# Kernel optimization log

Hardware: AMD Instinct MI355X
Metric: run time of the kernel (lower is better)

## Reference

```python
import jax, jax.numpy as jnp
import numpy as np

EPS = 1e-9  # Dice BatchNorm epsilon

def _dice(x, alpha, mm, mv):
    # Keras BN(center=False, scale=False) in inference mode: (x - moving_mean) / sqrt(moving_var + eps)
    p = jax.nn.sigmoid((x - mm) * jax.lax.rsqrt(mv + EPS))
    return x * (p + alpha * (1.0 - p))

def setup_inputs() -> dict:
    key = jax.random.key(0)
    ks = jax.random.split(key, 8)
    B, T, E = 4096, 200, 12
    return {
        "query": jax.random.normal(ks[0], (B, 1, E), jnp.float32),
        "keys": jax.random.normal(ks[1], (B, T, E), jnp.float32),
        "mask": jnp.ones((B, T), dtype=bool),
        "W0": jax.random.normal(ks[2], (48, 80), jnp.float32) * (1.0 / np.sqrt(48)),
        "b0": jnp.zeros((80,), jnp.float32),
        "W1": jax.random.normal(ks[3], (80, 40), jnp.float32) * (1.0 / np.sqrt(80)),
        "b1": jnp.zeros((40,), jnp.float32),
        "alpha0": jax.random.uniform(ks[4], (80,), jnp.float32),
        "alpha1": jax.random.uniform(ks[5], (40,), jnp.float32),
        "mm0": jnp.zeros((80,), jnp.float32),
        "mv0": jnp.ones((80,), jnp.float32),
        "mm1": jnp.zeros((40,), jnp.float32),
        "mv1": jnp.ones((40,), jnp.float32),
        "atten_kernel": jax.random.normal(ks[6], (40, 1), jnp.float32) * (1.0 / np.sqrt(40)),
        "atten_bias": jnp.zeros((1,), jnp.float32),
    }

def reference(query, keys, mask, W0, b0, W1, b1, alpha0, alpha1,
              mm0, mv0, mm1, mv1, atten_kernel, atten_bias):
    B, T, E = keys.shape
    q = jnp.broadcast_to(query, (B, T, E))  # K.repeat_elements(query, T, 1)
    att = jnp.concatenate([q, keys, q - keys, q * keys], axis=-1)  # [B, T, 4E=48]
    h = _dice(jnp.einsum('bti,io->bto', att, W0) + b0, alpha0, mm0, mv0)  # [B,T,80]
    h = _dice(jnp.einsum('bti,io->bto', h, W1) + b1, alpha1, mm1, mv1)    # [B,T,40]
    score = jnp.einsum('bti,io->bto', h, atten_kernel) + atten_bias       # [B,T,1]
    scores = jnp.swapaxes(score, 1, 2)  # [B,1,T]
    # NOTE: original code computes tf.where(mask,...) but overwrites it and
    # matmuls the UNMASKED scores with keys (bug reproduced faithfully).
    return jnp.matmul(scores, keys)  # [B,1,E]
```

## Files before the change

kernel.cpp:

```cpp
#include <hip/hip_runtime.h>
#include <hip/hip_bf16.h>
#include <math.h>

#define B_TOT 4096
#define T_LEN 200
#define E_DIM 12
#define LOG2E 1.44269504088896340736f

typedef __attribute__((ext_vector_type(8))) short bf16x8;
typedef __attribute__((ext_vector_type(4))) float f32x4;
typedef unsigned short ushort_t;


__device__ inline unsigned short f2bf(float f) {
    union { float f; unsigned u; } x; x.f = f;
    unsigned r = x.u + 0x7FFFu + ((x.u >> 16) & 1u);
    return (unsigned short)(r >> 16);
}
__device__ inline unsigned pk_bf16(float a, float b) {
    float2 t; t.x = a; t.y = b;
    __hip_bfloat162 h = __float22bfloat162_rn(t);
    union { __hip_bfloat162 h; unsigned u; } cv; cv.h = h;
    return cv.u;
}

__global__ __launch_bounds__(256) void din_prep(
    const float* __restrict__ W0, const float* __restrict__ b0v,
    const float* __restrict__ W1, const float* __restrict__ b1v,
    const float* __restrict__ a0, const float* __restrict__ a1,
    const float* __restrict__ mm0, const float* __restrict__ mv0,
    const float* __restrict__ mm1, const float* __restrict__ mv1,
    const float* __restrict__ ak, const float* __restrict__ ab,
    void* __restrict__ wsv)
{
    unsigned char* wsb = (unsigned char*)wsv;
    ushort_t* w0e2 = (ushort_t*)wsb;
    ushort_t* wq   = (ushort_t*)(wsb + 5120);
    ushort_t* w1e  = (ushort_t*)(wsb + 10240);
    float* d0c = (float*)(wsb + 19456);
    float* d1c = (float*)(wsb + 20736);

    int idx = blockIdx.x * 256 + threadIdx.x;
    if (idx < 2560) {
        int n = idx >> 5, k = idx & 31;
        float v = 0.0f;
        if (k < 12)       v = W0[(12 + k) * 80 + n] - W0[(24 + k) * 80 + n];
        else if (k < 24)  v = W0[(36 + (k - 12)) * 80 + n];
        w0e2[n * 32 + k] = f2bf(v);
    } else if (idx < 5120) {
        int v2 = idx - 2560;
        int n = v2 >> 5, k = v2 & 31;
        float v = 0.0f;
        if (k < 12)       v = W0[k * 80 + n] + W0[(24 + k) * 80 + n];
        else if (k == 12) v = b0v[n];
        wq[n * 32 + k] = f2bf(v);
    } else if (idx < 9728) {
        int v2 = idx - 5120;
        int n = v2 / 96, k = v2 - n * 96;
        float v = 0.0f;
        if (n < 40) {
            if (k < 80)       v = W1[k * 40 + n];
            else if (k == 80) v = b1v[n];
        } else if (n == 40 && k == 80) {
            v = 1.0f;
        }
        w1e[n * 96 + k] = f2bf(v);
    } else if (idx < 10048) {
        int v2 = idx - 9728;
        int o = v2 >> 2, c = v2 & 3;
        float rs = rsqrtf(mv0[o] + 1e-9f) * LOG2E;
        float val = (c == 0) ? -rs : (c == 1) ? mm0[o] * rs : (c == 2) ? a0[o] : 1.0f - a0[o];
        d0c[o * 4 + c] = val;
    } else {
        int v2 = idx - 10048;
        int j = v2 >> 2, c = v2 & 3;
        float val = 0.0f;
        if (j < 40) {
            float rs = rsqrtf(mv1[j] + 1e-9f) * LOG2E;
            val = (c == 0) ? -rs : (c == 1) ? mm1[j] * rs : (c == 2) ? a1[j] * ak[j]
                                                          : (1.0f - a1[j]) * ak[j];
        } else if (j == 40 && c == 2) {
            val = ab[0];
        }
        d1c[j * 4 + c] = val;
    }
}

#define A0_STR 40
#define H_STR  104
#define W1_STR 104
#define W0_STR 40

__global__ __launch_bounds__(256, 3) void din_mfma(
    const float* __restrict__ query, const float* __restrict__ keys,
    const void* __restrict__ wsv, float* __restrict__ out)
{
    __shared__ __align__(16) ushort_t Aseg[4 * 64];
    __shared__ __align__(16) ushort_t A0[4 * 64 * A0_STR];
    __shared__ __align__(16) ushort_t H[4 * 16 * H_STR];
    __shared__ __align__(16) f32x4 d0cL[80];
    __shared__ __align__(16) f32x4 d1cL[48];
    __shared__ __align__(16) ushort_t w1eL[48 * W1_STR];
    __shared__ __align__(16) ushort_t w0e2L[80 * W0_STR];
    const unsigned char* wsb = (const unsigned char*)wsv;
    const ushort_t* w0e2 = (const ushort_t*)wsb;
    const ushort_t* wq   = (const ushort_t*)(wsb + 5120);
    const ushort_t* w1e  = (const ushort_t*)(wsb + 10240);
    const f32x4* d0cp = (const f32x4*)(wsb + 19456);
    const f32x4* d1cp = (const f32x4*)(wsb + 20736);

    const int tid = threadIdx.x;
    const int lane = tid & 63;
    const int w = tid >> 6;
    const int l15 = lane & 15;
    const int quad = lane >> 4;
    const int b = blockIdx.x * 4 + w;

    ushort_t* A0w = &A0[w * 64 * A0_STR];
    ushort_t* Hw  = &H[w * 16 * H_STR];
    ushort_t* Asw = &Aseg[w * 64];

    if (tid < 80)        d0cL[tid] = d0cp[tid];
    else if (tid < 128)  d1cL[tid - 80] = d1cp[tid - 80];
    for (int idx = tid; idx < 48 * 12; idx += 256) {
        int row = idx / 12, g = idx - row * 12;
        *(uint4*)(w1eL + row * W1_STR + g * 8) =
            *(const uint4*)(w1e + row * 96 + g * 8);
    }
    for (int idx = tid; idx < 80 * 4; idx += 256) {
        int row = idx >> 2, g = idx & 3;
        *(uint4*)(w0e2L + row * W0_STR + g * 8) =
            *(const uint4*)(w0e2 + row * 32 + g * 8);
    }

    float qq[12];
    {
        const float4* qp = (const float4*)(query + (size_t)b * E_DIM);
        float4 q0 = qp[0], q1 = qp[1], q2 = qp[2];
        qq[0]=q0.x; qq[1]=q0.y; qq[2]=q0.z; qq[3]=q0.w;
        qq[4]=q1.x; qq[5]=q1.y; qq[6]=q1.z; qq[7]=q1.w;
        qq[8]=q2.x; qq[9]=q2.y; qq[10]=q2.z; qq[11]=q2.w;
    }

    float z0q[5];
    {
        unsigned p01 = pk_bf16(qq[0], qq[1]), p23 = pk_bf16(qq[2], qq[3]);
        unsigned p45 = pk_bf16(qq[4], qq[5]), p67 = pk_bf16(qq[6], qq[7]);
        unsigned p89 = pk_bf16(qq[8], qq[9]), pab = pk_bf16(qq[10], qq[11]);
        union { unsigned u[4]; bf16x8 v; } qa;
        qa.u[0] = (quad == 0) ? p01 : (quad == 1) ? p89 : 0u;
        qa.u[1] = (quad == 0) ? p23 : (quad == 1) ? pab : 0u;
        qa.u[2] = (quad == 0) ? p45 : (quad == 1) ? 0x00003F80u : 0u;
        qa.u[3] = (quad == 0) ? p67 : 0u;
        #pragma unroll
        for (int nt = 0; nt < 5; ++nt) {
            bf16x8 wf = *(const bf16x8*)(wq + (nt * 16 + l15) * 32 + quad * 8);
            f32x4 zz = {0.f, 0.f, 0.f, 0.f};
            zz = __builtin_amdgcn_mfma_f32_16x16x32_bf16(qa.v, wf, zz, 0, 0, 0);
            z0q[nt] = zz[0];
        }
    }

    if (quad == 0) {
        bf16x8 one8 = {(short)0x3F80, 0, 0, 0, 0, 0, 0, 0};
        bf16x8 zero8 = {0, 0, 0, 0, 0, 0, 0, 0};
        *(bf16x8*)(Hw + l15 * H_STR + 80) = one8;
        *(bf16x8*)(Hw + l15 * H_STR + 88) = zero8;
    }
    {
        uint4 z4; z4.x = 0u; z4.y = 0u; z4.z = 0u; z4.w = 0u;
        ((uint4*)(A0w + lane * A0_STR))[3] = z4;
    }

    __syncthreads();

    f32x4 acc2 = {0.f, 0.f, 0.f, 0.f};

    for (int c = 0; c < 4; ++c) {
        const int t0 = c * 64;
        const int myT = t0 + lane;
        const bool valid = myT < T_LEN;

        float kk[12];
        if (valid) {
            const float4* kp = (const float4*)(keys + ((size_t)b * T_LEN + myT) * E_DIM);
            float4 k0 = kp[0], k1 = kp[1], k2 = kp[2];
            kk[0]=k0.x; kk[1]=k0.y; kk[2]=k0.z; kk[3]=k0.w;
            kk[4]=k1.x; kk[5]=k1.y; kk[6]=k1.z; kk[7]=k1.w;
            kk[8]=k2.x; kk[9]=k2.y; kk[10]=k2.z; kk[11]=k2.w;
        } else {
            #pragma unroll
            for (int i = 0; i < 12; ++i) kk[i] = 0.0f;
        }
        {
            unsigned kw[6], qkw[6];
            #pragma unroll
            for (int i = 0; i < 6; ++i)
                kw[i] = pk_bf16(kk[2 * i], kk[2 * i + 1]);
            #pragma unroll
            for (int i = 0; i < 6; ++i)
                qkw[i] = pk_bf16(qq[2 * i] * kk[2 * i], qq[2 * i + 1] * kk[2 * i + 1]);
            uint4* dst = (uint4*)(A0w + lane * A0_STR);
            uint4 v0, v1, v2;
            v0.x = kw[0];  v0.y = kw[1];  v0.z = kw[2];  v0.w = kw[3];
            v1.x = kw[4];  v1.y = kw[5];  v1.z = qkw[0]; v1.w = qkw[1];
            v2.x = qkw[2]; v2.y = qkw[3]; v2.z = qkw[4]; v2.w = qkw[5];
            dst[0] = v0; dst[1] = v1; dst[2] = v2;
        }

        const int ntiles = (c < 3) ? 4 : 1;
        for (int ti = 0; ti < ntiles; ++ti) {
            bf16x8 a0 = *(const bf16x8*)(A0w + (ti * 16 + l15) * A0_STR + quad * 8);

            #pragma unroll
            for (int nt = 0; nt < 5; ++nt) {
                bf16x8 b0 = *(const bf16x8*)(w0e2L + (nt * 16 + l15) * W0_STR + quad * 8);
                float zq = z0q[nt];
                f32x4 cc = {zq, zq, zq, zq};
                cc = __builtin_amdgcn_mfma_f32_16x16x32_bf16(a0, b0, cc, 0, 0, 0);
                f32x4 dc = d0cL[nt * 16 + l15];
                float h[4];
                #pragma unroll
                for (int r = 0; r < 4; ++r) {
                    float z = cc[r];
                    float pg = __builtin_amdgcn_rcpf(
                        1.0f + __builtin_amdgcn_exp2f(fmaf(z, dc.x, dc.y)));
                    h[r] = z * fmaf(pg, dc.w, dc.z);
                }
                unsigned u01 = pk_bf16(h[0], h[1]);
                unsigned u23 = pk_bf16(h[2], h[3]);
                ushort_t* hcol = Hw + (quad * 4) * H_STR + nt * 16 + l15;
                hcol[0 * H_STR] = (ushort_t)u01;
                hcol[1 * H_STR] = (ushort_t)(u01 >> 16);
                hcol[2 * H_STR] = (ushort_t)u23;
                hcol[3 * H_STR] = (ushort_t)(u23 >> 16);
            }

            bf16x8 af[3];
            #pragma unroll
            for (int ks = 0; ks < 3; ++ks)
                af[ks] = *(const bf16x8*)(Hw + l15 * H_STR + ks * 32 + quad * 8);
            float s[4] = {0.f, 0.f, 0.f, 0.f};
            #pragma unroll
            for (int nt = 0; nt < 3; ++nt) {
                f32x4 cc = {0.f, 0.f, 0.f, 0.f};
                #pragma unroll
                for (int ks = 0; ks < 3; ++ks) {
                    bf16x8 bf = *(const bf16x8*)(w1eL + (nt * 16 + l15) * W1_STR
                                                 + ks * 32 + quad * 8);
                    cc = __builtin_amdgcn_mfma_f32_16x16x32_bf16(af[ks], bf, cc, 0, 0, 0);
                }
                f32x4 dc1 = d1cL[nt * 16 + l15];
                #pragma unroll
                for (int r = 0; r < 4; ++r) {
                    float z = cc[r];
                    float pg = __builtin_amdgcn_rcpf(
                        1.0f + __builtin_amdgcn_exp2f(fmaf(z, dc1.x, dc1.y)));
                    s[r] = fmaf(z, fmaf(pg, dc1.w, dc1.z), s[r]);
                }
            }
            #pragma unroll
            for (int m = 1; m < 16; m <<= 1) {
                #pragma unroll
                for (int r = 0; r < 4; ++r) s[r] += __shfl_xor(s[r], m, 64);
            }
            if (l15 == 0) {
                const int tb = t0 + ti * 16 + quad * 4;
                float v0 = (tb + 0 < T_LEN) ? s[0] : 0.0f;
                float v1 = (tb + 1 < T_LEN) ? s[1] : 0.0f;
                float v2 = (tb + 2 < T_LEN) ? s[2] : 0.0f;
                float v3 = (tb + 3 < T_LEN) ? s[3] : 0.0f;
                unsigned lo = pk_bf16(v0, v1), hi = pk_bf16(v2, v3);
                unsigned long long pk = (unsigned long long)lo
                                      | ((unsigned long long)hi << 32);
                *(unsigned long long*)(Asw + ti * 16 + quad * 4) = pk;
            }
        }

        const int nks = (c < 3) ? 2 : 1;
        for (int ks = 0; ks < nks; ++ks) {
            bf16x8 pa = *(const bf16x8*)(Asw + l15 * 64 + ks * 32 + quad * 8);
            bf16x8 bk;
            #pragma unroll
            for (int j = 0; j < 8; ++j)
                bk[j] = (short)A0w[(ks * 32 + quad * 8 + j) * A0_STR + l15];
            acc2 = __builtin_amdgcn_mfma_f32_16x16x32_bf16(pa, bk, acc2, 0, 0, 0);
        }
    }

    if (quad == 0 && l15 < 12)
        out[(size_t)b * E_DIM + l15] = acc2[0];
}

extern "C" void kernel_launch(void* const* d_in, const int* in_sizes, int n_in,
                              void* d_out, int out_size, void* d_ws, size_t ws_size,
                              hipStream_t stream) {
    const float* query = (const float*)d_in[0];
    const float* keys  = (const float*)d_in[1];
    const float* W0  = (const float*)d_in[3];
    const float* b0v = (const float*)d_in[4];
    const float* W1  = (const float*)d_in[5];
    const float* b1v = (const float*)d_in[6];
    const float* a0  = (const float*)d_in[7];
    const float* a1  = (const float*)d_in[8];
    const float* mm0 = (const float*)d_in[9];
    const float* mv0 = (const float*)d_in[10];
    const float* mm1 = (const float*)d_in[11];
    const float* mv1 = (const float*)d_in[12];
    const float* ak  = (const float*)d_in[13];
    const float* ab  = (const float*)d_in[14];
    float* out = (float*)d_out;

    hipLaunchKernelGGL(din_prep, dim3(40), dim3(256), 0, stream,
                       W0, b0v, W1, b1v, a0, a1, mm0, mv0, mm1, mv1, ak, ab, d_ws);
    hipLaunchKernelGGL(din_mfma, dim3(B_TOT / 4), dim3(256), 0, stream,
                       query, keys, d_ws, out);
}
```

Baseline: 151.1 us.

## Fuse weight-prep kernel into main kernel, building packed weights per block

Removes the separate prep kernel. Each block of the main kernel now builds its bf16 weight tiles and Dice constants in shared memory directly from the raw fp32 parameters. The query projection is also changed from a small MFMA over packed bf16 weights to a scalar fp32 FMA loop reading W0 from global memory. This saves one launch and the workspace round trip, but every one of the 1024 blocks repeats the prep work with scattered, uncoalesced W0/W1 reads.

Result: slower. 164.5 us (+8.9%).

```diff
diff --git a/kernel.cpp b/kernel.cpp
--- a/kernel.cpp
+++ b/kernel.cpp
@@ -10,7 +10,6 @@
 typedef __attribute__((ext_vector_type(8))) short bf16x8;
 typedef __attribute__((ext_vector_type(4))) float f32x4;
 typedef unsigned short ushort_t;
-
 
 __device__ inline unsigned short f2bf(float f) {
     union { float f; unsigned u; } x; x.f = f;
@@ -24,76 +23,20 @@
     return cv.u;
 }
 
-__global__ __launch_bounds__(256) void din_prep(
-    const float* __restrict__ W0, const float* __restrict__ b0v,
-    const float* __restrict__ W1, const float* __restrict__ b1v,
-    const float* __restrict__ a0, const float* __restrict__ a1,
-    const float* __restrict__ mm0, const float* __restrict__ mv0,
-    const float* __restrict__ mm1, const float* __restrict__ mv1,
-    const float* __restrict__ ak, const float* __restrict__ ab,
-    void* __restrict__ wsv)
-{
-    unsigned char* wsb = (unsigned char*)wsv;
-    ushort_t* w0e2 = (ushort_t*)wsb;
-    ushort_t* wq   = (ushort_t*)(wsb + 5120);
-    ushort_t* w1e  = (ushort_t*)(wsb + 10240);
-    float* d0c = (float*)(wsb + 19456);
-    float* d1c = (float*)(wsb + 20736);
-
-    int idx = blockIdx.x * 256 + threadIdx.x;
-    if (idx < 2560) {
-        int n = idx >> 5, k = idx & 31;
-        float v = 0.0f;
-        if (k < 12)       v = W0[(12 + k) * 80 + n] - W0[(24 + k) * 80 + n];
-        else if (k < 24)  v = W0[(36 + (k - 12)) * 80 + n];
-        w0e2[n * 32 + k] = f2bf(v);
-    } else if (idx < 5120) {
-        int v2 = idx - 2560;
-        int n = v2 >> 5, k = v2 & 31;
-        float v = 0.0f;
-        if (k < 12)       v = W0[k * 80 + n] + W0[(24 + k) * 80 + n];
-        else if (k == 12) v = b0v[n];
-        wq[n * 32 + k] = f2bf(v);
-    } else if (idx < 9728) {
-        int v2 = idx - 5120;
-        int n = v2 / 96, k = v2 - n * 96;
-        float v = 0.0f;
-        if (n < 40) {
-            if (k < 80)       v = W1[k * 40 + n];
-            else if (k == 80) v = b1v[n];
-        } else if (n == 40 && k == 80) {
-            v = 1.0f;
-        }
-        w1e[n * 96 + k] = f2bf(v);
-    } else if (idx < 10048) {
-        int v2 = idx - 9728;
-        int o = v2 >> 2, c = v2 & 3;
-        float rs = rsqrtf(mv0[o] + 1e-9f) * LOG2E;
-        float val = (c == 0) ? -rs : (c == 1) ? mm0[o] * rs : (c == 2) ? a0[o] : 1.0f - a0[o];
-        d0c[o * 4 + c] = val;
-    } else {
-        int v2 = idx - 10048;
-        int j = v2 >> 2, c = v2 & 3;
-        float val = 0.0f;
-        if (j < 40) {
-            float rs = rsqrtf(mv1[j] + 1e-9f) * LOG2E;
-            val = (c == 0) ? -rs : (c == 1) ? mm1[j] * rs : (c == 2) ? a1[j] * ak[j]
-                                                          : (1.0f - a1[j]) * ak[j];
-        } else if (j == 40 && c == 2) {
-            val = ab[0];
-        }
-        d1c[j * 4 + c] = val;
-    }
-}
-
 #define A0_STR 40
 #define H_STR  104
 #define W1_STR 104
 #define W0_STR 40
 
-__global__ __launch_bounds__(256, 3) void din_mfma(
+__global__ __launch_bounds__(256, 3) void din_fused(
     const float* __restrict__ query, const float* __restrict__ keys,
-    const void* __restrict__ wsv, float* __restrict__ out)
+    const float* __restrict__ W0, const float* __restrict__ b0v,
+    const float* __restrict__ W1, const float* __restrict__ b1v,
+    const float* __restrict__ a0v, const float* __restrict__ a1v,
+    const float* __restrict__ mm0, const float* __restrict__ mv0,
+    const float* __restrict__ mm1, const float* __restrict__ mv1,
+    const float* __restrict__ akp, const float* __restrict__ abp,
+    float* __restrict__ out)
 {
     __shared__ __align__(16) ushort_t Aseg[4 * 64];
     __shared__ __align__(16) ushort_t A0[4 * 64 * A0_STR];
@@ -102,12 +45,6 @@
     __shared__ __align__(16) f32x4 d1cL[48];
     __shared__ __align__(16) ushort_t w1eL[48 * W1_STR];
     __shared__ __align__(16) ushort_t w0e2L[80 * W0_STR];
-    const unsigned char* wsb = (const unsigned char*)wsv;
-    const ushort_t* w0e2 = (const ushort_t*)wsb;
-    const ushort_t* wq   = (const ushort_t*)(wsb + 5120);
-    const ushort_t* w1e  = (const ushort_t*)(wsb + 10240);
-    const f32x4* d0cp = (const f32x4*)(wsb + 19456);
-    const f32x4* d1cp = (const f32x4*)(wsb + 20736);
 
     const int tid = threadIdx.x;
     const int lane = tid & 63;
@@ -120,17 +57,40 @@
     ushort_t* Hw  = &H[w * 16 * H_STR];
     ushort_t* Asw = &Aseg[w * 64];
 
-    if (tid < 80)        d0cL[tid] = d0cp[tid];
-    else if (tid < 128)  d1cL[tid - 80] = d1cp[tid - 80];
-    for (int idx = tid; idx < 48 * 12; idx += 256) {
-        int row = idx / 12, g = idx - row * 12;
-        *(uint4*)(w1eL + row * W1_STR + g * 8) =
-            *(const uint4*)(w1e + row * 96 + g * 8);
-    }
-    for (int idx = tid; idx < 80 * 4; idx += 256) {
-        int row = idx >> 2, g = idx & 3;
-        *(uint4*)(w0e2L + row * W0_STR + g * 8) =
-            *(const uint4*)(w0e2 + row * 32 + g * 8);
+    for (int idx = tid; idx < 80 * 32; idx += 256) {
+        int n = idx >> 5, k = idx & 31;
+        float v = 0.0f;
+        if (k < 12)       v = W0[(12 + k) * 80 + n] - W0[(24 + k) * 80 + n];
+        else if (k < 24)  v = W0[(36 + (k - 12)) * 80 + n];
+        w0e2L[n * W0_STR + k] = f2bf(v);
+    }
+    for (int idx = tid; idx < 48 * 96; idx += 256) {
+        int n = idx / 96, k = idx - n * 96;
+        float v = 0.0f;
+        if (n < 40) {
+            if (k < 80)       v = W1[k * 40 + n];
+            else if (k == 80) v = b1v[n];
+        } else if (n == 40 && k == 80) {
+            v = 1.0f;
+        }
+        w1eL[n * W1_STR + k] = f2bf(v);
+    }
+    for (int o = tid; o < 80; o += 256) {
+        float rs = rsqrtf(mv0[o] + 1e-9f) * LOG2E;
+        f32x4 dv; dv.x = -rs; dv.y = mm0[o] * rs; dv.z = a0v[o]; dv.w = 1.0f - a0v[o];
+        d0cL[o] = dv;
+    }
+    if (tid < 48) {
+        int j = tid;
+        f32x4 dv; dv.x = 0.f; dv.y = 0.f; dv.z = 0.f; dv.w = 0.f;
+        if (j < 40) {
+            float rs = rsqrtf(mv1[j] + 1e-9f) * LOG2E;
+            dv.x = -rs; dv.y = mm1[j] * rs;
+            dv.z = a1v[j] * akp[j]; dv.w = (1.0f - a1v[j]) * akp[j];
+        } else if (j == 40) {
+            dv.z = abp[0];
+        }
+        d1cL[j] = dv;
     }
 
     float qq[12];
@@ -143,22 +103,14 @@
     }
 
     float z0q[5];
-    {
-        unsigned p01 = pk_bf16(qq[0], qq[1]), p23 = pk_bf16(qq[2], qq[3]);
-        unsigned p45 = pk_bf16(qq[4], qq[5]), p67 = pk_bf16(qq[6], qq[7]);
-        unsigned p89 = pk_bf16(qq[8], qq[9]), pab = pk_bf16(qq[10], qq[11]);
-        union { unsigned u[4]; bf16x8 v; } qa;
-        qa.u[0] = (quad == 0) ? p01 : (quad == 1) ? p89 : 0u;
-        qa.u[1] = (quad == 0) ? p23 : (quad == 1) ? pab : 0u;
-        qa.u[2] = (quad == 0) ? p45 : (quad == 1) ? 0x00003F80u : 0u;
-        qa.u[3] = (quad == 0) ? p67 : 0u;
+    #pragma unroll
+    for (int nt = 0; nt < 5; ++nt) {
+        int n = nt * 16 + l15;
+        float z = b0v[n];
         #pragma unroll
-        for (int nt = 0; nt < 5; ++nt) {
-            bf16x8 wf = *(const bf16x8*)(wq + (nt * 16 + l15) * 32 + quad * 8);
-            f32x4 zz = {0.f, 0.f, 0.f, 0.f};
-            zz = __builtin_amdgcn_mfma_f32_16x16x32_bf16(qa.v, wf, zz, 0, 0, 0);
-            z0q[nt] = zz[0];
-        }
+        for (int i = 0; i < 12; ++i)
+            z = fmaf(qq[i], W0[i * 80 + n] + W0[(24 + i) * 80 + n], z);
+        z0q[nt] = z;
     }
 
     if (quad == 0) {
@@ -311,8 +263,7 @@
     const float* ab  = (const float*)d_in[14];
     float* out = (float*)d_out;
 
-    hipLaunchKernelGGL(din_prep, dim3(40), dim3(256), 0, stream,
-                       W0, b0v, W1, b1v, a0, a1, mm0, mv0, mm1, mv1, ak, ab, d_ws);
-    hipLaunchKernelGGL(din_mfma, dim3(B_TOT / 4), dim3(256), 0, stream,
-                       query, keys, d_ws, out);
-}
+    hipLaunchKernelGGL(din_fused, dim3(B_TOT / 4), dim3(256), 0, stream,
+                       query, keys, W0, b0v, W1, b1v, a0, a1,
+                       mm0, mv0, mm1, mv1, ak, ab, out);
+}
```
